# Kernel tuning notes

Measured on AMD Instinct MI355X. Metric: run time of the kernel, lower is better.

The kernel has to match this reference:

```python
import jax, jax.numpy as jnp
import numpy as np

ENC_DIM, DEC_DIM, ATT_DIM = 2048, 512, 512
B, N = 256, 196


def setup_inputs() -> dict:
    key = jax.random.key(0)
    ks = jax.random.split(key, 8)
    s_enc = 1.0 / np.sqrt(ENC_DIM)
    s_dec = 1.0 / np.sqrt(DEC_DIM)
    s_full = 1.0 / np.sqrt(ATT_DIM)
    return {
        "encoder_out": jax.random.normal(ks[0], (B, N, ENC_DIM), jnp.float32),
        "hidden": jax.random.normal(ks[1], (B, DEC_DIM), jnp.float32),
        "W_enc": jax.random.uniform(ks[2], (ENC_DIM, ATT_DIM), jnp.float32, -s_enc, s_enc),
        "b_enc": jax.random.uniform(ks[3], (ATT_DIM,), jnp.float32, -s_enc, s_enc),
        "W_dec": jax.random.uniform(ks[4], (DEC_DIM, ATT_DIM), jnp.float32, -s_dec, s_dec),
        "b_dec": jax.random.uniform(ks[5], (ATT_DIM,), jnp.float32, -s_dec, s_dec),
        "W_full": jax.random.uniform(ks[6], (ATT_DIM, 1), jnp.float32, -s_full, s_full),
        "b_full": jax.random.uniform(ks[7], (1,), jnp.float32, -s_full, s_full),
    }


def reference(encoder_out, hidden, W_enc, b_enc, W_dec, b_dec, W_full, b_full):
    # enc proj: [B, N, A]; dec proj: [B, 1, A] broadcast over pixels
    att1 = jnp.einsum('bne,ea->bna', encoder_out, W_enc) + b_enc
    att2 = hidden @ W_dec + b_dec                       # [B, A]
    att = jax.nn.relu(att1 + att2[:, None, :])          # [B, N, A]
    scores = (jnp.einsum('bna,a->bn', att, W_full[:, 0]) + b_full[0])  # [B, N]
    alpha = jax.nn.softmax(scores, axis=1)              # softmax over pixels
    context = jnp.einsum('bne,bn->be', encoder_out, alpha)  # [B, E]
    return (context, alpha)
```

## Files before the change

### kernel.cpp

```cpp
#include <hip/hip_runtime.h>
#include <hip/hip_bf16.h>
#include <stdint.h>

#define ENC_DIM 2048
#define ATT_DIM 512
#define BATCH   256
#define NPIX    196
#define MROWS   (BATCH*NPIX)
#define CTX_OFF (BATCH*ENC_DIM)
#define KC      64
#define NCH     (ENC_DIM/KC)

typedef __attribute__((ext_vector_type(8))) short  short8;
typedef __attribute__((ext_vector_type(4))) float  f32x4;

__device__ __forceinline__ uint32_t f2bf(float x) {
    union { float f; uint32_t u; } v; v.f = x;
    return (v.u + 0x7FFFu + ((v.u >> 16) & 1u)) >> 16;
}

__device__ __forceinline__ uint4 pack8(f32x4 a0, f32x4 a1) {
    uint4 u;
    u.x = f2bf(a0[0]) | (f2bf(a0[1]) << 16);
    u.y = f2bf(a0[2]) | (f2bf(a0[3]) << 16);
    u.z = f2bf(a1[0]) | (f2bf(a1[1]) << 16);
    u.w = f2bf(a1[2]) | (f2bf(a1[3]) << 16);
    return u;
}

__global__ __launch_bounds__(256) void pack_wenc(const float* __restrict__ W,
                                                 unsigned short* __restrict__ Wp) {
    const int i  = blockIdx.x * 256 + threadIdx.x;
    const int n  = i & 511;
    const int kg = i >> 9;
    short8 v;
#pragma unroll
    for (int j = 0; j < 8; ++j)
        v[j] = (short)f2bf(W[(size_t)(kg * 8 + j) * 512 + n]);
    *(short8*)(Wp + (size_t)i * 8) = v;
}

__global__ __launch_bounds__(256) void att2_kernel(const float* __restrict__ hidden,
                                                   const float* __restrict__ Wdec,
                                                   const float* __restrict__ bdec,
                                                   const float* __restrict__ benc,
                                                   float* __restrict__ att2p) {
    __shared__ float h[512];
    const int b   = blockIdx.x;
    const int tid = threadIdx.x;
    h[tid]       = hidden[(size_t)b * 512 + tid];
    h[tid + 256] = hidden[(size_t)b * 512 + tid + 256];
    __syncthreads();
    float acc0 = bdec[tid]       + benc[tid];
    float acc1 = bdec[tid + 256] + benc[tid + 256];
#pragma unroll 4
    for (int k = 0; k < 512; ++k) {
        const float hk = h[k];
        acc0 = fmaf(hk, Wdec[(size_t)k * 512 + tid],       acc0);
        acc1 = fmaf(hk, Wdec[(size_t)k * 512 + tid + 256], acc1);
    }
    att2p[(size_t)b * 512 + tid]       = acc0;
    att2p[(size_t)b * 512 + tid + 256] = acc1;
}

__global__ __launch_bounds__(512, 3) void score_kernel(const float* __restrict__ enc,
                                                       const unsigned short* __restrict__ Wp,
                                                       const float* __restrict__ att2p,
                                                       const float* __restrict__ Wfull,
                                                       float* __restrict__ scores) {
    __shared__ __align__(16) unsigned char ldsA[2][64 * KC * 2];
    __shared__ float lds_att2[2][ATT_DIM];
    __shared__ float lds_wf[ATT_DIM];
    __shared__ float lds_sc[64];

    const int tid = threadIdx.x;
    const int w   = tid >> 6;
    const int l   = tid & 63;
    const int m0  = blockIdx.x * 64;
    const int b0  = m0 / NPIX;
    const int b1  = (m0 + 63) / NPIX;

    lds_att2[0][tid] = att2p[(size_t)b0 * ATT_DIM + tid];
    lds_att2[1][tid] = att2p[(size_t)b1 * ATT_DIM + tid];
    lds_wf[tid] = Wfull[tid];
    if (tid < 64) lds_sc[tid] = 0.0f;

    const int arow = tid >> 3;
    const int akg  = tid & 7;
    const int awr  = arow * 128 + ((akg ^ (arow & 7)) << 4);
    const float* aG = enc + (size_t)(m0 + arow) * ENC_DIM + akg * 8;

    int ard[4], akey[4];
#pragma unroll
    for (int mf = 0; mf < 4; ++mf) {
        const int r = mf * 16 + (l & 15);
        ard[mf]  = r * 128;
        akey[mf] = r & 7;
    }
    const int kq = l >> 4;

    int boff[4];
#pragma unroll
    for (int nf = 0; nf < 4; ++nf)
        boff[nf] = (kq * 512 + (w << 6) + (nf << 4) + (l & 15)) * 8;

    f32x4 acc[4][4];
#pragma unroll
    for (int i = 0; i < 4; ++i)
#pragma unroll
        for (int j = 0; j < 4; ++j)
            acc[i][j] = (f32x4){0.f, 0.f, 0.f, 0.f};

    {
        f32x4 a0 = *(const f32x4*)aG;
        f32x4 a1 = *(const f32x4*)(aG + 4);
        *(uint4*)(ldsA[0] + awr) = pack8(a0, a1);
    }
    f32x4 rc0 = *(const f32x4*)(aG + KC);
    f32x4 rc1 = *(const f32x4*)(aG + KC + 4);
    __syncthreads();

#define STEP(S, BV)                                                            \
    {                                                                          \
        _Pragma("unroll")                                                      \
        for (int mf = 0; mf < 4; ++mf) {                                       \
            short8 af = *(const short8*)(ldsR + ard[mf] +                      \
                                         ((((S) * 4 + kq) ^ akey[mf]) << 4));  \
            _Pragma("unroll")                                                  \
            for (int nf = 0; nf < 4; ++nf)                                     \
                acc[mf][nf] = __builtin_amdgcn_mfma_f32_16x16x32_bf16(         \
                    af, BV[nf], acc[mf][nf], 0, 0, 0);                         \
        }                                                                      \
    }

#pragma unroll 1
    for (int c = 0; c < NCH; ++c) {
        const int p = c & 1;
        const unsigned char* ldsR = ldsA[p];
        const unsigned short* bC  = Wp + (size_t)c * 32768;
        short8 b0v[4], b1v[4];
#pragma unroll
        for (int nf = 0; nf < 4; ++nf) b0v[nf] = *(const short8*)(bC + boff[nf]);
#pragma unroll
        for (int nf = 0; nf < 4; ++nf) b1v[nf] = *(const short8*)(bC + boff[nf] + 16384);
        const int cc = (c + 2 < NCH) ? (c + 2) : (NCH - 1);
        f32x4 rn0 = *(const f32x4*)(aG + cc * KC);
        f32x4 rn1 = *(const f32x4*)(aG + cc * KC + 4);
        STEP(0, b0v)
        if (c + 1 < NCH)
            *(uint4*)(ldsA[p ^ 1] + awr) = pack8(rc0, rc1);
        STEP(1, b1v)
        asm volatile("s_waitcnt lgkmcnt(0)" ::: "memory");
        __builtin_amdgcn_s_barrier();
        rc0 = rn0; rc1 = rn1;
    }
#undef STEP

#pragma unroll
    for (int mf = 0; mf < 4; ++mf) {
#pragma unroll
        for (int reg = 0; reg < 4; ++reg) {
            const int row = mf * 16 + ((l >> 4) << 2) + reg;
            const int sel = ((m0 + row) >= (b0 + 1) * NPIX) ? 1 : 0;
            float sv = 0.0f;
#pragma unroll
            for (int nf = 0; nf < 4; ++nf) {
                const int col = (w << 6) + (nf << 4) + (l & 15);
                float v = acc[mf][nf][reg] + lds_att2[sel][col];
                v = fmaxf(v, 0.0f);
                sv = fmaf(v, lds_wf[col], sv);
            }
            sv += __shfl_xor(sv, 8);
            sv += __shfl_xor(sv, 4);
            sv += __shfl_xor(sv, 2);
            sv += __shfl_xor(sv, 1);
            if ((l & 15) == 0) atomicAdd(&lds_sc[row], sv);
        }
    }
    __syncthreads();
    if (tid < 64) scores[m0 + tid] = lds_sc[tid];
}

__global__ __launch_bounds__(256) void ctx_kernel(const float* __restrict__ enc,
                                                  const float* __restrict__ scores,
                                                  float* __restrict__ out) {
    __shared__ float salpha[NPIX];
    __shared__ float red[8];
    __shared__ float partial[512];
    const int tid  = threadIdx.x;
    const int lane = tid & 63;
    const int wid  = tid >> 6;
    const int b    = blockIdx.x >> 2;
    const int eq   = blockIdx.x & 3;

    const float sv = (tid < NPIX) ? scores[(size_t)b * NPIX + tid] : -1e30f;
    float mx = sv;
#pragma unroll
    for (int m = 32; m >= 1; m >>= 1) mx = fmaxf(mx, __shfl_xor(mx, m));
    if (lane == 0) red[wid] = mx;
    __syncthreads();
    if (tid == 0) red[4] = fmaxf(fmaxf(red[0], red[1]), fmaxf(red[2], red[3]));
    __syncthreads();
    const float bm = red[4];
    const float ex = (tid < NPIX) ? __expf(sv - bm) : 0.0f;
    float sm = ex;
#pragma unroll
    for (int m = 32; m >= 1; m >>= 1) sm += __shfl_xor(sm, m);
    if (lane == 0) red[wid] = sm;
    __syncthreads();
    if (tid == 0) red[5] = red[0] + red[1] + red[2] + red[3];
    __syncthreads();
    const float inv = 1.0f / red[5];
    if (tid < NPIX) {
        const float av = ex * inv;
        salpha[tid] = av;
        if (eq == 0) out[CTX_OFF + (size_t)b * NPIX + tid] = av;
    }
    __syncthreads();

    const int l128 = tid & 127;
    const int ph   = tid >> 7;
    const float* ep = enc + (size_t)b * NPIX * ENC_DIM + eq * 512 + l128 * 4;
    f32x4 acc = (f32x4){0.f, 0.f, 0.f, 0.f};
#pragma unroll 4
    for (int n = ph; n < NPIX; n += 2) {
        const float al = salpha[n];
        f32x4 v = *(const f32x4*)(ep + (size_t)n * ENC_DIM);
        acc += v * al;
    }
    if (ph == 1) *(f32x4*)(partial + l128 * 4) = acc;
    __syncthreads();
    if (ph == 0) {
        f32x4 o = acc + *(const f32x4*)(partial + l128 * 4);
        *(f32x4*)(out + (size_t)b * ENC_DIM + eq * 512 + l128 * 4) = o;
    }
}

extern "C" void kernel_launch(void* const* d_in, const int* in_sizes, int n_in,
                              void* d_out, int out_size, void* d_ws, size_t ws_size,
                              hipStream_t stream) {
    const float* enc    = (const float*)d_in[0];
    const float* hidden = (const float*)d_in[1];
    const float* Wenc   = (const float*)d_in[2];
    const float* benc   = (const float*)d_in[3];
    const float* Wdec   = (const float*)d_in[4];
    const float* bdec   = (const float*)d_in[5];
    const float* Wfull  = (const float*)d_in[6];
    float* out = (float*)d_out;

    unsigned short* Wp    = (unsigned short*)d_ws;
    float*          att2p = (float*)((char*)d_ws + (2u << 20));
    float*          scores= (float*)((char*)d_ws + (2u << 20) + (512u << 10));

    pack_wenc   <<<512, 256, 0, stream>>>(Wenc, Wp);
    att2_kernel <<<BATCH, 256, 0, stream>>>(hidden, Wdec, bdec, benc, att2p);
    score_kernel<<<MROWS / 64, 512, 0, stream>>>(enc, Wp, att2p, Wfull, scores);
    ctx_kernel  <<<BATCH * 4, 256, 0, stream>>>(enc, scores, out);
}
```

Before: 296.4 us.

## Compute transposed score GEMM with direct register loads, dropping LDS staging

The score GEMM is restructured to compute W_enc^T x enc^T. The weight is repacked transposed (A rows = attention dims) and read straight from global/L2 as MFMA A fragments. Encoder rows are loaded per lane, converted to bf16 in registers and used as B fragments, so the LDS double buffer and per-chunk barriers go away. Each wave now owns 128 attention dims by 32 pixels. The epilogue reduction changes to match. The trade-off is that weight fragments are re-read from global/L2 by every wave without LDS sharing, and the global loads are less coalesced, so latency may be less well hidden.

```diff
diff --git a/kernel.cpp b/kernel.cpp
--- a/kernel.cpp
+++ b/kernel.cpp
@@ -8,8 +8,6 @@
 #define NPIX    196
 #define MROWS   (BATCH*NPIX)
 #define CTX_OFF (BATCH*ENC_DIM)
-#define KC      64
-#define NCH     (ENC_DIM/KC)
 
 typedef __attribute__((ext_vector_type(8))) short  short8;
 typedef __attribute__((ext_vector_type(4))) float  f32x4;
@@ -19,25 +17,25 @@
     return (v.u + 0x7FFFu + ((v.u >> 16) & 1u)) >> 16;
 }
 
-__device__ __forceinline__ uint4 pack8(f32x4 a0, f32x4 a1) {
-    uint4 u;
-    u.x = f2bf(a0[0]) | (f2bf(a0[1]) << 16);
-    u.y = f2bf(a0[2]) | (f2bf(a0[3]) << 16);
-    u.z = f2bf(a1[0]) | (f2bf(a1[1]) << 16);
-    u.w = f2bf(a1[2]) | (f2bf(a1[3]) << 16);
-    return u;
-}
-
-__global__ __launch_bounds__(256) void pack_wenc(const float* __restrict__ W,
-                                                 unsigned short* __restrict__ Wp) {
+__device__ __forceinline__ short8 cvt8(f32x4 x, f32x4 y) {
+    short8 r;
+    r[0] = (short)f2bf(x[0]); r[1] = (short)f2bf(x[1]);
+    r[2] = (short)f2bf(x[2]); r[3] = (short)f2bf(x[3]);
+    r[4] = (short)f2bf(y[0]); r[5] = (short)f2bf(y[1]);
+    r[6] = (short)f2bf(y[2]); r[7] = (short)f2bf(y[3]);
+    return r;
+}
+
+__global__ __launch_bounds__(256) void pack_wt(const float* __restrict__ W,
+                                               unsigned short* __restrict__ Wt) {
     const int i  = blockIdx.x * 256 + threadIdx.x;
-    const int n  = i & 511;
-    const int kg = i >> 9;
+    const int a  = i >> 8;
+    const int kg = i & 255;
     short8 v;
 #pragma unroll
     for (int j = 0; j < 8; ++j)
-        v[j] = (short)f2bf(W[(size_t)(kg * 8 + j) * 512 + n]);
-    *(short8*)(Wp + (size_t)i * 8) = v;
+        v[j] = (short)f2bf(W[(size_t)(kg * 8 + j) * 512 + a]);
+    *(short8*)(Wt + (size_t)a * 2048 + kg * 8) = v;
 }
 
 __global__ __launch_bounds__(256) void att2_kernel(const float* __restrict__ hidden,
@@ -64,11 +62,10 @@
 }
 
 __global__ __launch_bounds__(512, 3) void score_kernel(const float* __restrict__ enc,
-                                                       const unsigned short* __restrict__ Wp,
+                                                       const unsigned short* __restrict__ Wt,
                                                        const float* __restrict__ att2p,
                                                        const float* __restrict__ Wfull,
                                                        float* __restrict__ scores) {
-    __shared__ __align__(16) unsigned char ldsA[2][64 * KC * 2];
     __shared__ float lds_att2[2][ATT_DIM];
     __shared__ float lds_wf[ATT_DIM];
     __shared__ float lds_sc[64];
@@ -76,6 +73,8 @@
     const int tid = threadIdx.x;
     const int w   = tid >> 6;
     const int l   = tid & 63;
+    const int ag  = w & 3;
+    const int pg  = w >> 2;
     const int m0  = blockIdx.x * 64;
     const int b0  = m0 / NPIX;
     const int b1  = (m0 + 63) / NPIX;
@@ -84,98 +83,65 @@
     lds_att2[1][tid] = att2p[(size_t)b1 * ATT_DIM + tid];
     lds_wf[tid] = Wfull[tid];
     if (tid < 64) lds_sc[tid] = 0.0f;
-
-    const int arow = tid >> 3;
-    const int akg  = tid & 7;
-    const int awr  = arow * 128 + ((akg ^ (arow & 7)) << 4);
-    const float* aG = enc + (size_t)(m0 + arow) * ENC_DIM + akg * 8;
-
-    int ard[4], akey[4];
-#pragma unroll
-    for (int mf = 0; mf < 4; ++mf) {
-        const int r = mf * 16 + (l & 15);
-        ard[mf]  = r * 128;
-        akey[mf] = r & 7;
-    }
-    const int kq = l >> 4;
-
-    int boff[4];
-#pragma unroll
-    for (int nf = 0; nf < 4; ++nf)
-        boff[nf] = (kq * 512 + (w << 6) + (nf << 4) + (l & 15)) * 8;
-
-    f32x4 acc[4][4];
-#pragma unroll
-    for (int i = 0; i < 4; ++i)
-#pragma unroll
-        for (int j = 0; j < 4; ++j)
-            acc[i][j] = (f32x4){0.f, 0.f, 0.f, 0.f};
-
-    {
-        f32x4 a0 = *(const f32x4*)aG;
-        f32x4 a1 = *(const f32x4*)(aG + 4);
-        *(uint4*)(ldsA[0] + awr) = pack8(a0, a1);
-    }
-    f32x4 rc0 = *(const f32x4*)(aG + KC);
-    f32x4 rc1 = *(const f32x4*)(aG + KC + 4);
-    __syncthreads();
-
-#define STEP(S, BV)                                                            \
-    {                                                                          \
-        _Pragma("unroll")                                                      \
-        for (int mf = 0; mf < 4; ++mf) {                                       \
-            short8 af = *(const short8*)(ldsR + ard[mf] +                      \
-                                         ((((S) * 4 + kq) ^ akey[mf]) << 4));  \
-            _Pragma("unroll")                                                  \
-            for (int nf = 0; nf < 4; ++nf)                                     \
-                acc[mf][nf] = __builtin_amdgcn_mfma_f32_16x16x32_bf16(         \
-                    af, BV[nf], acc[mf][nf], 0, 0, 0);                         \
-        }                                                                      \
-    }
+    __syncthreads();
+
+    const int lr = l & 15;
+    const int ko = l >> 4;
+
+    const unsigned short* pA = Wt + ((size_t)(ag * 128 + lr)) * 2048 + ko * 8;
+    const float* pB0 = enc + ((size_t)(m0 + pg * 32 + lr)) * ENC_DIM + ko * 8;
+    const float* pB1 = pB0 + (size_t)16 * ENC_DIM;
+
+    f32x4 acc[8][2];
+#pragma unroll
+    for (int i = 0; i < 8; ++i) {
+        acc[i][0] = (f32x4){0.f, 0.f, 0.f, 0.f};
+        acc[i][1] = (f32x4){0.f, 0.f, 0.f, 0.f};
+    }
+
+    f32x4 b0a = *(const f32x4*)(pB0);
+    f32x4 b0b = *(const f32x4*)(pB0 + 4);
+    f32x4 b1a = *(const f32x4*)(pB1);
+    f32x4 b1b = *(const f32x4*)(pB1 + 4);
 
 #pragma unroll 1
-    for (int c = 0; c < NCH; ++c) {
-        const int p = c & 1;
-        const unsigned char* ldsR = ldsA[p];
-        const unsigned short* bC  = Wp + (size_t)c * 32768;
-        short8 b0v[4], b1v[4];
-#pragma unroll
-        for (int nf = 0; nf < 4; ++nf) b0v[nf] = *(const short8*)(bC + boff[nf]);
-#pragma unroll
-        for (int nf = 0; nf < 4; ++nf) b1v[nf] = *(const short8*)(bC + boff[nf] + 16384);
-        const int cc = (c + 2 < NCH) ? (c + 2) : (NCH - 1);
-        f32x4 rn0 = *(const f32x4*)(aG + cc * KC);
-        f32x4 rn1 = *(const f32x4*)(aG + cc * KC + 4);
-        STEP(0, b0v)
-        if (c + 1 < NCH)
-            *(uint4*)(ldsA[p ^ 1] + awr) = pack8(rc0, rc1);
-        STEP(1, b1v)
-        asm volatile("s_waitcnt lgkmcnt(0)" ::: "memory");
-        __builtin_amdgcn_s_barrier();
-        rc0 = rn0; rc1 = rn1;
-    }
-#undef STEP
-
-#pragma unroll
-    for (int mf = 0; mf < 4; ++mf) {
-#pragma unroll
-        for (int reg = 0; reg < 4; ++reg) {
-            const int row = mf * 16 + ((l >> 4) << 2) + reg;
-            const int sel = ((m0 + row) >= (b0 + 1) * NPIX) ? 1 : 0;
-            float sv = 0.0f;
-#pragma unroll
-            for (int nf = 0; nf < 4; ++nf) {
-                const int col = (w << 6) + (nf << 4) + (l & 15);
-                float v = acc[mf][nf][reg] + lds_att2[sel][col];
+    for (int s = 0; s < 64; ++s) {
+        const short8 bf0 = cvt8(b0a, b0b);
+        const short8 bf1 = cvt8(b1a, b1b);
+        if (s < 63) {
+            const int off = (s + 1) * 32;
+            b0a = *(const f32x4*)(pB0 + off);
+            b0b = *(const f32x4*)(pB0 + off + 4);
+            b1a = *(const f32x4*)(pB1 + off);
+            b1b = *(const f32x4*)(pB1 + off + 4);
+        }
+        const unsigned short* pAs = pA + s * 32;
+#pragma unroll
+        for (int af = 0; af < 8; ++af) {
+            const short8 avf = *(const short8*)(pAs + (size_t)af * 32768);
+            acc[af][0] = __builtin_amdgcn_mfma_f32_16x16x32_bf16(avf, bf0, acc[af][0], 0, 0, 0);
+            acc[af][1] = __builtin_amdgcn_mfma_f32_16x16x32_bf16(avf, bf1, acc[af][1], 0, 0, 0);
+        }
+    }
+
+#pragma unroll
+    for (int pf = 0; pf < 2; ++pf) {
+        const int pix = pg * 32 + pf * 16 + lr;
+        const int sel = ((m0 + pix) >= (b0 + 1) * NPIX) ? 1 : 0;
+        float sp = 0.0f;
+#pragma unroll
+        for (int af = 0; af < 8; ++af) {
+#pragma unroll
+            for (int r = 0; r < 4; ++r) {
+                const int a = ag * 128 + af * 16 + ko * 4 + r;
+                float v = acc[af][pf][r] + lds_att2[sel][a];
                 v = fmaxf(v, 0.0f);
-                sv = fmaf(v, lds_wf[col], sv);
+                sp = fmaf(v, lds_wf[a], sp);
             }
-            sv += __shfl_xor(sv, 8);
-            sv += __shfl_xor(sv, 4);
-            sv += __shfl_xor(sv, 2);
-            sv += __shfl_xor(sv, 1);
-            if ((l & 15) == 0) atomicAdd(&lds_sc[row], sv);
         }
+        sp += __shfl_xor(sp, 16);
+        sp += __shfl_xor(sp, 32);
+        if (l < 16) atomicAdd(&lds_sc[pg * 32 + pf * 16 + l], sp);
     }
     __syncthreads();
     if (tid < 64) scores[m0 + tid] = lds_sc[tid];
@@ -248,12 +214,12 @@
     const float* Wfull  = (const float*)d_in[6];
     float* out = (float*)d_out;
 
-    unsigned short* Wp    = (unsigned short*)d_ws;
+    unsigned short* Wt    = (unsigned short*)d_ws;
     float*          att2p = (float*)((char*)d_ws + (2u << 20));
     float*          scores= (float*)((char*)d_ws + (2u << 20) + (512u << 10));
 
-    pack_wenc   <<<512, 256, 0, stream>>>(Wenc, Wp);
+    pack_wt     <<<512, 256, 0, stream>>>(Wenc, Wt);
     att2_kernel <<<BATCH, 256, 0, stream>>>(hidden, Wdec, bdec, benc, att2p);
-    score_kernel<<<MROWS / 64, 512, 0, stream>>>(enc, Wp, att2p, Wfull, scores);
+    score_kernel<<<MROWS / 64, 512, 0, stream>>>(enc, Wt, att2p, Wfull, scores);
     ctx_kernel  <<<BATCH * 4, 256, 0, stream>>>(enc, scores, out);
 }
```

Measured after the change: 831.6 us. 181% more time.

## Split score GEMM N dimension across two blocks with atomic score accumulation

Applied to the files above, without the earlier changes.

The score kernel now launches two 256-thread blocks per 64-row tile, each covering half of the 512 attention columns. Partial scores are combined with global atomicAdd into a buffer that a new kernel zeroes first. The aim is more blocks and better occupancy and load balance across CUs. The cost is that each encoder tile is read and converted to bf16 twice, plus an extra launch and global atomics.

```diff
diff --git a/kernel.cpp b/kernel.cpp
--- a/kernel.cpp
+++ b/kernel.cpp
@@ -10,6 +10,7 @@
 #define CTX_OFF (BATCH*ENC_DIM)
 #define KC      64
 #define NCH     (ENC_DIM/KC)
+#define NPAIR   784
 
 typedef __attribute__((ext_vector_type(8))) short  short8;
 typedef __attribute__((ext_vector_type(4))) float  f32x4;
@@ -63,7 +64,11 @@
     att2p[(size_t)b * 512 + tid + 256] = acc1;
 }
 
-__global__ __launch_bounds__(512, 3) void score_kernel(const float* __restrict__ enc,
+__global__ __launch_bounds__(256) void zero_scores(float* __restrict__ scores) {
+    scores[blockIdx.x * 256 + threadIdx.x] = 0.0f;
+}
+
+__global__ __launch_bounds__(256, 3) void score_kernel(const float* __restrict__ enc,
                                                        const unsigned short* __restrict__ Wp,
                                                        const float* __restrict__ att2p,
                                                        const float* __restrict__ Wfull,
@@ -73,36 +78,41 @@
     __shared__ float lds_wf[ATT_DIM];
     __shared__ float lds_sc[64];
 
-    const int tid = threadIdx.x;
-    const int w   = tid >> 6;
-    const int l   = tid & 63;
-    const int m0  = blockIdx.x * 64;
-    const int b0  = m0 / NPIX;
-    const int b1  = (m0 + 63) / NPIX;
-
-    lds_att2[0][tid] = att2p[(size_t)b0 * ATT_DIM + tid];
-    lds_att2[1][tid] = att2p[(size_t)b1 * ATT_DIM + tid];
-    lds_wf[tid] = Wfull[tid];
+    const int tid  = threadIdx.x;
+    const int w    = tid >> 6;
+    const int l    = tid & 63;
+    const int lr   = l & 15;
+    const int kq   = l >> 4;
+    const int pair = blockIdx.x % NPAIR;
+    const int half = blockIdx.x / NPAIR;
+    const int m0   = pair * 64;
+    const int b0   = m0 / NPIX;
+    const int b1   = (m0 + 63) / NPIX;
+
+    lds_att2[0][tid]       = att2p[(size_t)b0 * ATT_DIM + tid];
+    lds_att2[0][tid + 256] = att2p[(size_t)b0 * ATT_DIM + tid + 256];
+    lds_att2[1][tid]       = att2p[(size_t)b1 * ATT_DIM + tid];
+    lds_att2[1][tid + 256] = att2p[(size_t)b1 * ATT_DIM + tid + 256];
+    lds_wf[tid]       = Wfull[tid];
+    lds_wf[tid + 256] = Wfull[tid + 256];
     if (tid < 64) lds_sc[tid] = 0.0f;
 
-    const int arow = tid >> 3;
-    const int akg  = tid & 7;
-    const int awr  = arow * 128 + ((akg ^ (arow & 7)) << 4);
-    const float* aG = enc + (size_t)(m0 + arow) * ENC_DIM + akg * 8;
-
-    int ard[4], akey[4];
-#pragma unroll
-    for (int mf = 0; mf < 4; ++mf) {
-        const int r = mf * 16 + (l & 15);
-        ard[mf]  = r * 128;
-        akey[mf] = r & 7;
-    }
-    const int kq = l >> 4;
+    const int arow = tid >> 2;
+    const int aj   = tid & 3;
+    const int key  = arow & 7;
+    const int aw0  = arow * 128 + (((aj * 2)     ^ key) << 4);
+    const int aw1  = arow * 128 + (((aj * 2 + 1) ^ key) << 4);
+    const float* aG = enc + (size_t)(m0 + arow) * ENC_DIM + aj * 16;
+
+    int ard[4];
+#pragma unroll
+    for (int mf = 0; mf < 4; ++mf) ard[mf] = (mf * 16 + lr) * 128;
+    const int akey = l & 7;
 
     int boff[4];
 #pragma unroll
     for (int nf = 0; nf < 4; ++nf)
-        boff[nf] = (kq * 512 + (w << 6) + (nf << 4) + (l & 15)) * 8;
+        boff[nf] = (kq * 512 + half * 256 + (w << 6) + (nf << 4) + lr) * 8;
 
     f32x4 acc[4][4];
 #pragma unroll
@@ -112,12 +122,17 @@
             acc[i][j] = (f32x4){0.f, 0.f, 0.f, 0.f};
 
     {
-        f32x4 a0 = *(const f32x4*)aG;
-        f32x4 a1 = *(const f32x4*)(aG + 4);
-        *(uint4*)(ldsA[0] + awr) = pack8(a0, a1);
+        f32x4 s0 = *(const f32x4*)(aG);
+        f32x4 s1 = *(const f32x4*)(aG + 4);
+        f32x4 s2 = *(const f32x4*)(aG + 8);
+        f32x4 s3 = *(const f32x4*)(aG + 12);
+        *(uint4*)(ldsA[0] + aw0) = pack8(s0, s1);
+        *(uint4*)(ldsA[0] + aw1) = pack8(s2, s3);
     }
     f32x4 rc0 = *(const f32x4*)(aG + KC);
     f32x4 rc1 = *(const f32x4*)(aG + KC + 4);
+    f32x4 rc2 = *(const f32x4*)(aG + KC + 8);
+    f32x4 rc3 = *(const f32x4*)(aG + KC + 12);
     __syncthreads();
 
 #define STEP(S, BV)                                                            \
@@ -125,7 +140,7 @@
         _Pragma("unroll")                                                      \
         for (int mf = 0; mf < 4; ++mf) {                                       \
             short8 af = *(const short8*)(ldsR + ard[mf] +                      \
-                                         ((((S) * 4 + kq) ^ akey[mf]) << 4));  \
+                                         ((((S) * 4 + kq) ^ akey) << 4));      \
             _Pragma("unroll")                                                  \
             for (int nf = 0; nf < 4; ++nf)                                     \
                 acc[mf][nf] = __builtin_amdgcn_mfma_f32_16x16x32_bf16(         \
@@ -146,13 +161,17 @@
         const int cc = (c + 2 < NCH) ? (c + 2) : (NCH - 1);
         f32x4 rn0 = *(const f32x4*)(aG + cc * KC);
         f32x4 rn1 = *(const f32x4*)(aG + cc * KC + 4);
+        f32x4 rn2 = *(const f32x4*)(aG + cc * KC + 8);
+        f32x4 rn3 = *(const f32x4*)(aG + cc * KC + 12);
         STEP(0, b0v)
-        if (c + 1 < NCH)
-            *(uint4*)(ldsA[p ^ 1] + awr) = pack8(rc0, rc1);
+        if (c + 1 < NCH) {
+            *(uint4*)(ldsA[p ^ 1] + aw0) = pack8(rc0, rc1);
+            *(uint4*)(ldsA[p ^ 1] + aw1) = pack8(rc2, rc3);
+        }
         STEP(1, b1v)
         asm volatile("s_waitcnt lgkmcnt(0)" ::: "memory");
         __builtin_amdgcn_s_barrier();
-        rc0 = rn0; rc1 = rn1;
+        rc0 = rn0; rc1 = rn1; rc2 = rn2; rc3 = rn3;
     }
 #undef STEP
 
@@ -160,12 +179,12 @@
     for (int mf = 0; mf < 4; ++mf) {
 #pragma unroll
         for (int reg = 0; reg < 4; ++reg) {
-            const int row = mf * 16 + ((l >> 4) << 2) + reg;
+            const int row = mf * 16 + (kq << 2) + reg;
             const int sel = ((m0 + row) >= (b0 + 1) * NPIX) ? 1 : 0;
             float sv = 0.0f;
 #pragma unroll
             for (int nf = 0; nf < 4; ++nf) {
-                const int col = (w << 6) + (nf << 4) + (l & 15);
+                const int col = half * 256 + (w << 6) + (nf << 4) + lr;
                 float v = acc[mf][nf][reg] + lds_att2[sel][col];
                 v = fmaxf(v, 0.0f);
                 sv = fmaf(v, lds_wf[col], sv);
@@ -174,11 +193,11 @@
             sv += __shfl_xor(sv, 4);
             sv += __shfl_xor(sv, 2);
             sv += __shfl_xor(sv, 1);
-            if ((l & 15) == 0) atomicAdd(&lds_sc[row], sv);
+            if (lr == 0) atomicAdd(&lds_sc[row], sv);
         }
     }
     __syncthreads();
-    if (tid < 64) scores[m0 + tid] = lds_sc[tid];
+    if (tid < 64) atomicAdd(&scores[m0 + tid], lds_sc[tid]);
 }
 
 __global__ __launch_bounds__(256) void ctx_kernel(const float* __restrict__ enc,
@@ -254,6 +273,7 @@
 
     pack_wenc   <<<512, 256, 0, stream>>>(Wenc, Wp);
     att2_kernel <<<BATCH, 256, 0, stream>>>(hidden, Wdec, bdec, benc, att2p);
-    score_kernel<<<MROWS / 64, 512, 0, stream>>>(enc, Wp, att2p, Wfull, scores);
+    zero_scores <<<MROWS / 256, 256, 0, stream>>>(scores);
+    score_kernel<<<2 * NPAIR, 256, 0, stream>>>(enc, Wp, att2p, Wfull, scores);
     ctx_kernel  <<<BATCH * 4, 256, 0, stream>>>(enc, scores, out);
 }
```

Result: slower. 372.1 us (+25.6%).
